# Optimization experiments

Hardware: AMD Instinct MI355X
Metric: run time of the kernel (lower is better)

The kernel has to match this reference:

```python
import jax, jax.numpy as jnp
import numpy as np

TOP_K = 2


def setup_inputs() -> dict:
    key = jax.random.key(0)
    ks = jax.random.split(key, 5)
    B, N, C, FF, E = 2, 2048, 1024, 4096, 8
    x = jax.random.normal(ks[0], (B, N, C), dtype=jnp.float32)
    router_w = jax.random.normal(ks[1], (E, C), dtype=jnp.float32) * 0.02
    # xavier-uniform-like init for expert weights
    lim1 = np.sqrt(6.0 / (FF + C))
    expert_w1 = jax.random.uniform(ks[2], (E, FF, C), dtype=jnp.float32, minval=-lim1, maxval=lim1)
    expert_b1 = jnp.zeros((E, FF), dtype=jnp.float32)
    expert_w2 = jax.random.uniform(ks[3], (E, C, FF), dtype=jnp.float32, minval=-lim1, maxval=lim1)
    expert_b2 = jnp.zeros((E, C), dtype=jnp.float32)
    return {"x": x, "router_w": router_w, "expert_w1": expert_w1,
            "expert_b1": expert_b1, "expert_w2": expert_w2, "expert_b2": expert_b2}


def reference(x, router_w, expert_w1, expert_b1, expert_w2, expert_b2):
    # x: [B,N,C]; router_w: [E,C]; expert_w1: [E,FF,C]; expert_w2: [E,C,FF]
    router_logits = jnp.einsum('bnc,ec->bne', x, router_w)          # [B,N,E]
    router_probs = jax.nn.softmax(router_logits, axis=-1)
    expert_weights, expert_idx = jax.lax.top_k(router_probs, TOP_K)  # [B,N,K]
    expert_weights = expert_weights / (expert_weights.sum(axis=-1, keepdims=True) + 1e-9)
    # Dense all-expert FFN (avoids materializing per-token gathered weight matrices)
    h = jnp.einsum('bnc,efc->bnef', x, expert_w1) + expert_b1        # [B,N,E,FF]
    h = jax.nn.gelu(h, approximate=False)                            # torch nn.GELU = exact
    out_all = jnp.einsum('bnef,ecf->bnec', h, expert_w2) + expert_b2  # [B,N,E,C]
    # Gather top-k expert outputs and combine
    out_k = jnp.take_along_axis(out_all, expert_idx[..., None], axis=2)  # [B,N,K,C]
    return (out_k * expert_weights[..., None]).sum(axis=2)           # [B,N,C]
```

## Files before the change

### kernel.cpp

```cpp
#include <hip/hip_runtime.h>
#include <hip/hip_bf16.h>
#include <cstdint>

#define TTOK  4096
#define CDIM  1024
#define FFDIM 4096
#define NEXP  8


typedef short short8 __attribute__((ext_vector_type(8)));
typedef float f32x4 __attribute__((ext_vector_type(4)));

__device__ __forceinline__ unsigned short f2bf(float f) {
    unsigned int u = __float_as_uint(f);
    u = u + 0x7fffu + ((u >> 16) & 1u);
    return (unsigned short)(u >> 16);
}

__device__ __forceinline__ void gl_lds16(const unsigned short* g, unsigned short* l) {
    __builtin_amdgcn_global_load_lds(
        (const __attribute__((address_space(1))) unsigned int*)g,
        (__attribute__((address_space(3))) unsigned int*)l, 16, 0, 0);
}

__device__ __forceinline__ int swz_off(int row, int kq) {
    const int line = row >> 1;
    const int cp = ((((row & 1) << 2) | kq) ^ (line & 7));
    return line * 64 + cp * 8;
}

#define SBAR() do { __builtin_amdgcn_sched_barrier(0); \
                    __builtin_amdgcn_s_barrier();      \
                    __builtin_amdgcn_sched_barrier(0); } while (0)

__global__ void cast_kernel(const float* __restrict__ src, unsigned short* __restrict__ dst) {
    int i = blockIdx.x * blockDim.x + threadIdx.x;
    float4 v = reinterpret_cast<const float4*>(src)[i];
    ushort4 o;
    o.x = f2bf(v.x); o.y = f2bf(v.y); o.z = f2bf(v.z); o.w = f2bf(v.w);
    reinterpret_cast<ushort4*>(dst)[i] = o;
}

__global__ void router_kernel(const float* __restrict__ x, const float* __restrict__ rw,
                              int* __restrict__ counts, int* __restrict__ btok,
                              float* __restrict__ bgate) {
    const int wave = threadIdx.x >> 6;
    const int lane = threadIdx.x & 63;
    const int t = blockIdx.x * 4 + wave;
    const float* xr = x + (size_t)t * CDIM;

    float acc[NEXP];
#pragma unroll
    for (int e = 0; e < NEXP; e++) acc[e] = 0.f;
    for (int c = lane; c < CDIM; c += 64) {
        float xv = xr[c];
#pragma unroll
        for (int e = 0; e < NEXP; e++) acc[e] += xv * rw[e * CDIM + c];
    }
#pragma unroll
    for (int e = 0; e < NEXP; e++) {
#pragma unroll
        for (int off = 32; off > 0; off >>= 1) acc[e] += __shfl_down(acc[e], off, 64);
    }
    if (lane == 0) {
        float mx = acc[0];
#pragma unroll
        for (int e = 1; e < NEXP; e++) mx = fmaxf(mx, acc[e]);
        float p[NEXP]; float s = 0.f;
#pragma unroll
        for (int e = 0; e < NEXP; e++) { p[e] = expf(acc[e] - mx); s += p[e]; }
        int i0 = 0;
#pragma unroll
        for (int e = 1; e < NEXP; e++) if (p[e] > p[i0]) i0 = e;
        int i1 = (i0 == 0) ? 1 : 0;
#pragma unroll
        for (int e = 0; e < NEXP; e++) if (e != i0 && p[e] > p[i1]) i1 = e;
        float pr0 = p[i0] / s, pr1 = p[i1] / s;
        float rs = 1.f / (pr0 + pr1 + 1e-9f);
        float w0 = pr0 * rs, w1 = pr1 * rs;
        int pos = atomicAdd(&counts[i0], 1);
        btok[i0 * TTOK + pos] = t; bgate[i0 * TTOK + pos] = w0;
        pos = atomicAdd(&counts[i1], 1);
        btok[i1 * TTOK + pos] = t; bgate[i1 * TTOK + pos] = w1;
    }
}

__global__ void offsets_kernel(const int* __restrict__ counts, int* __restrict__ offsets) {
    if (threadIdx.x == 0 && blockIdx.x == 0) {
        int s = 0;
        for (int e = 0; e < NEXP; e++) { offsets[e] = s; s += counts[e]; }
        offsets[NEXP] = s;
    }
}


__global__ __launch_bounds__(512, 2) void gemm1p_kernel(
    const unsigned short* __restrict__ xb, const unsigned short* __restrict__ w1b,
    const float* __restrict__ b1, const int* __restrict__ counts,
    const int* __restrict__ offsets, const int* __restrict__ btok,
    unsigned short* __restrict__ H) {
    const int e = blockIdx.z;
    const int cnt = counts[e];
    const int m0 = blockIdx.y * 256;
    if (m0 >= cnt) return;
    const int n0 = blockIdx.x * 256;
    const int po = offsets[e];
    const int NT = CDIM / 32;

    __shared__ uint4 smem4[8192];
    unsigned short* S = (unsigned short*)smem4;

    const int tid = threadIdx.x;
    const int wid = tid >> 6, lane = tid & 63;
    const int lm = lane & 15, kq = lane >> 4;
    const int wr = wid >> 2, wc = wid & 3;

    const int sline = tid >> 3;
    const int c128s = (tid & 7) ^ (sline & 7);
    const int prty  = c128s >> 2;
    const int skc   = (c128s & 3) << 3;
    const int ar0 = min(m0 + (sline << 1) + prty, cnt - 1);
    const int ar1 = min(m0 + 128 + (sline << 1) + prty, cnt - 1);
    const unsigned short* asrc0 = xb + (size_t)btok[e * TTOK + ar0] * CDIM + skc;
    const unsigned short* asrc1 = xb + (size_t)btok[e * TTOK + ar1] * CDIM + skc;
    const unsigned short* bsrc0 = w1b + ((size_t)e * FFDIM + n0 + (sline << 1) + prty) * CDIM + skc;
    const unsigned short* bsrc1 = bsrc0 + (size_t)128 * CDIM;

    int offA[8], offB[4];
#pragma unroll
    for (int f = 0; f < 8; f++) offA[f] = swz_off(wr * 128 + f * 16 + lm, kq);
#pragma unroll
    for (int g = 0; g < 4; g++) offB[g] = swz_off(wc * 64 + g * 16 + lm, kq);

    f32x4 acc[8][4];
#pragma unroll
    for (int f = 0; f < 8; f++)
#pragma unroll
        for (int g = 0; g < 4; g++) { f32x4 z = {0.f, 0.f, 0.f, 0.f}; acc[f][g] = z; }

#pragma unroll
    for (int tt = 0; tt < 3; tt++) {
        unsigned short* Sa = S + tt * 16384;
        unsigned short* Sb = Sa + 8192;
        const int ko = tt * 32;
        gl_lds16(asrc0 + ko, Sa + tid * 8);
        gl_lds16(bsrc0 + ko, Sb + tid * 8);
        gl_lds16(asrc1 + ko, Sa + (512 + tid) * 8);
        gl_lds16(bsrc1 + ko, Sb + (512 + tid) * 8);
    }
    asm volatile("s_waitcnt vmcnt(8)" ::: "memory");
    SBAR();

    for (int t = 0; t < NT; ++t) {
        unsigned short* Ab = S + (t & 3) * 16384;
        unsigned short* Bb = Ab + 8192;
        int ts = t + 3; if (ts >= NT) ts -= NT;
        unsigned short* Sa = S + (ts & 3) * 16384;
        unsigned short* Sb = Sa + 8192;
        const int ko = ts * 32;

        short8 bf[4];
        {
            short8 af[4];
#pragma unroll
            for (int f = 0; f < 4; f++) af[f] = *reinterpret_cast<const short8*>(&Ab[offA[f]]);
#pragma unroll
            for (int g = 0; g < 4; g++) bf[g] = *reinterpret_cast<const short8*>(&Bb[offB[g]]);
            gl_lds16(asrc0 + ko, Sa + tid * 8);
            gl_lds16(bsrc0 + ko, Sb + tid * 8);
            SBAR();
            __builtin_amdgcn_s_setprio(1);
#pragma unroll
            for (int f = 0; f < 4; f++)
#pragma unroll
                for (int g = 0; g < 4; g++)
                    acc[f][g] = __builtin_amdgcn_mfma_f32_16x16x32_bf16(af[f], bf[g], acc[f][g], 0, 0, 0);
            __builtin_amdgcn_s_setprio(0);
            SBAR();
        }
        {
            short8 af[4];
#pragma unroll
            for (int f = 0; f < 4; f++) af[f] = *reinterpret_cast<const short8*>(&Ab[offA[4 + f]]);
            gl_lds16(asrc1 + ko, Sa + (512 + tid) * 8);
            gl_lds16(bsrc1 + ko, Sb + (512 + tid) * 8);
            asm volatile("s_waitcnt vmcnt(8)" ::: "memory");
            SBAR();
            __builtin_amdgcn_s_setprio(1);
#pragma unroll
            for (int f = 0; f < 4; f++)
#pragma unroll
                for (int g = 0; g < 4; g++)
                    acc[4 + f][g] = __builtin_amdgcn_mfma_f32_16x16x32_bf16(af[f], bf[g], acc[4 + f][g], 0, 0, 0);
            __builtin_amdgcn_s_setprio(0);
            SBAR();
        }
    }

    asm volatile("s_waitcnt vmcnt(0)" ::: "memory");
    __syncthreads();

    float bias[4];
#pragma unroll
    for (int g = 0; g < 4; g++) bias[g] = b1[e * FFDIM + n0 + wc * 64 + g * 16 + lm];

    unsigned short* Cs = S;
#pragma unroll
    for (int f = 0; f < 8; f++) {
#pragma unroll
        for (int r = 0; r < 4; r++) {
            const int row = wr * 128 + f * 16 + kq * 4 + r;
#pragma unroll
            for (int g = 0; g < 4; g++) {
                const int col = wc * 64 + g * 16 + lm;
                float h = acc[f][g][r] + bias[g];
                float gl = 0.5f * h * (1.f + erff(h * 0.70710678118654752f));
                Cs[(row * 256 + col) ^ ((row & 7) << 3)] = f2bf(gl);
            }
        }
    }
    __syncthreads();
#pragma unroll
    for (int q = 0; q < 16; q++) {
        const int cq = q * 512 + tid;
        const int row = cq >> 5;
        const int cc = cq & 31;
        const int mrow = m0 + row;
        if (mrow < cnt)
            *reinterpret_cast<uint4*>(&H[(size_t)(po + mrow) * FFDIM + n0 + cc * 8]) =
                *reinterpret_cast<const uint4*>(&Cs[(row * 256 + cc * 8) ^ ((row & 7) << 3)]);
    }
}

__global__ __launch_bounds__(512, 2) void gemm2p_kernel(
    const unsigned short* __restrict__ H, const unsigned short* __restrict__ w2b,
    const float* __restrict__ b2, const int* __restrict__ counts,
    const int* __restrict__ offsets, const int* __restrict__ btok,
    const float* __restrict__ bgate, float* __restrict__ out) {
    const int e = blockIdx.z;
    const int cnt = counts[e];
    const int m0 = (blockIdx.y >> 1) * 256;
    const int ks = blockIdx.y & 1;
    if (m0 >= cnt) return;
    const int n0 = blockIdx.x * 256;
    const int po = offsets[e];
    const int NT = 2048 / 32;

    __shared__ uint4 smem4[8192];
    unsigned short* S = (unsigned short*)smem4;

    const int tid = threadIdx.x;
    const int wid = tid >> 6, lane = tid & 63;
    const int lm = lane & 15, kq = lane >> 4;
    const int wr = wid >> 2, wc = wid & 3;

    const int sline = tid >> 3;
    const int c128s = (tid & 7) ^ (sline & 7);
    const int prty  = c128s >> 2;
    const int skc   = (c128s & 3) << 3;
    const int koff  = ks * 2048;
    const int ar0 = min(m0 + (sline << 1) + prty, cnt - 1);
    const int ar1 = min(m0 + 128 + (sline << 1) + prty, cnt - 1);
    const unsigned short* asrc0 = H + (size_t)(po + ar0) * FFDIM + koff + skc;
    const unsigned short* asrc1 = H + (size_t)(po + ar1) * FFDIM + koff + skc;
    const unsigned short* bsrc0 = w2b + ((size_t)e * CDIM + n0 + (sline << 1) + prty) * FFDIM + koff + skc;
    const unsigned short* bsrc1 = bsrc0 + (size_t)128 * FFDIM;

    int offA[8], offB[4];
#pragma unroll
    for (int f = 0; f < 8; f++) offA[f] = swz_off(wr * 128 + f * 16 + lm, kq);
#pragma unroll
    for (int g = 0; g < 4; g++) offB[g] = swz_off(wc * 64 + g * 16 + lm, kq);

    f32x4 acc[8][4];
#pragma unroll
    for (int f = 0; f < 8; f++)
#pragma unroll
        for (int g = 0; g < 4; g++) { f32x4 z = {0.f, 0.f, 0.f, 0.f}; acc[f][g] = z; }

#pragma unroll
    for (int tt = 0; tt < 3; tt++) {
        unsigned short* Sa = S + tt * 16384;
        unsigned short* Sb = Sa + 8192;
        const int ko = tt * 32;
        gl_lds16(asrc0 + ko, Sa + tid * 8);
        gl_lds16(bsrc0 + ko, Sb + tid * 8);
        gl_lds16(asrc1 + ko, Sa + (512 + tid) * 8);
        gl_lds16(bsrc1 + ko, Sb + (512 + tid) * 8);
    }
    asm volatile("s_waitcnt vmcnt(8)" ::: "memory");
    SBAR();

    for (int t = 0; t < NT; ++t) {
        unsigned short* Ab = S + (t & 3) * 16384;
        unsigned short* Bb = Ab + 8192;
        int ts = t + 3; if (ts >= NT) ts -= NT;
        unsigned short* Sa = S + (ts & 3) * 16384;
        unsigned short* Sb = Sa + 8192;
        const int ko = ts * 32;

        short8 bf[4];
        {
            short8 af[4];
#pragma unroll
            for (int f = 0; f < 4; f++) af[f] = *reinterpret_cast<const short8*>(&Ab[offA[f]]);
#pragma unroll
            for (int g = 0; g < 4; g++) bf[g] = *reinterpret_cast<const short8*>(&Bb[offB[g]]);
            gl_lds16(asrc0 + ko, Sa + tid * 8);
            gl_lds16(bsrc0 + ko, Sb + tid * 8);
            SBAR();
            __builtin_amdgcn_s_setprio(1);
#pragma unroll
            for (int f = 0; f < 4; f++)
#pragma unroll
                for (int g = 0; g < 4; g++)
                    acc[f][g] = __builtin_amdgcn_mfma_f32_16x16x32_bf16(af[f], bf[g], acc[f][g], 0, 0, 0);
            __builtin_amdgcn_s_setprio(0);
            SBAR();
        }
        {
            short8 af[4];
#pragma unroll
            for (int f = 0; f < 4; f++) af[f] = *reinterpret_cast<const short8*>(&Ab[offA[4 + f]]);
            gl_lds16(asrc1 + ko, Sa + (512 + tid) * 8);
            gl_lds16(bsrc1 + ko, Sb + (512 + tid) * 8);
            asm volatile("s_waitcnt vmcnt(8)" ::: "memory");
            SBAR();
            __builtin_amdgcn_s_setprio(1);
#pragma unroll
            for (int f = 0; f < 4; f++)
#pragma unroll
                for (int g = 0; g < 4; g++)
                    acc[4 + f][g] = __builtin_amdgcn_mfma_f32_16x16x32_bf16(af[f], bf[g], acc[4 + f][g], 0, 0, 0);
            __builtin_amdgcn_s_setprio(0);
            SBAR();
        }
    }

    asm volatile("s_waitcnt vmcnt(0)" ::: "memory");

    float bias[4];
#pragma unroll
    for (int g = 0; g < 4; g++)
        bias[g] = (ks == 0) ? b2[e * CDIM + n0 + wc * 64 + g * 16 + lm] : 0.f;

#pragma unroll
    for (int f = 0; f < 8; f++) {
#pragma unroll
        for (int r = 0; r < 4; r++) {
            const int mrow = m0 + wr * 128 + f * 16 + kq * 4 + r;
            if (mrow < cnt) {
                const int tok = btok[e * TTOK + mrow];
                const float g8 = bgate[e * TTOK + mrow];
                float* orow = out + (size_t)tok * CDIM + n0;
#pragma unroll
                for (int g = 0; g < 4; g++)
                    atomicAdd(orow + wc * 64 + g * 16 + lm, g8 * (acc[f][g][r] + bias[g]));
            }
        }
    }
}


__global__ __launch_bounds__(256) void gemm1_kernel(
    const unsigned short* __restrict__ xb, const float* __restrict__ w1,
    const float* __restrict__ b1, const int* __restrict__ counts,
    const int* __restrict__ offsets, const int* __restrict__ btok,
    unsigned short* __restrict__ H) {
    const int e = blockIdx.z;
    const int cnt = counts[e];
    const int m0 = blockIdx.y * 128;
    if (m0 >= cnt) return;
    const int n0 = blockIdx.x * 128;
    const int po = offsets[e];

    __shared__ unsigned short As[128][32];
    __shared__ unsigned short Bs[128][32];

    const int tid = threadIdx.x;
    const int wave = tid >> 6, lane = tid & 63;
    const int wm = (wave >> 1) << 6, wn = (wave & 1) << 6;
    const int lm = lane & 15, kq = lane >> 4;

    f32x4 acc[4][4];
#pragma unroll
    for (int i = 0; i < 4; i++)
#pragma unroll
        for (int j = 0; j < 4; j++) { f32x4 z = {0.f, 0.f, 0.f, 0.f}; acc[i][j] = z; }

    const float* w1e = w1 + (size_t)e * FFDIM * CDIM;
    const int arow = tid >> 1;
    const int acolb = (tid & 1) * 16;
    int tokA = -1;
    if (m0 + arow < cnt) tokA = btok[e * TTOK + m0 + arow];
    const int brow = tid >> 1;
    const int bcol = (tid & 1) * 16;

    for (int k0 = 0; k0 < CDIM; k0 += 32) {
        uint4 a0 = {0, 0, 0, 0}, a1 = {0, 0, 0, 0};
        if (tokA >= 0) {
            const uint4* src = reinterpret_cast<const uint4*>(xb + (size_t)tokA * CDIM + k0 + acolb);
            a0 = src[0]; a1 = src[1];
        }
        *reinterpret_cast<uint4*>(&As[arow][acolb]) = a0;
        *reinterpret_cast<uint4*>(&As[arow][acolb + 8]) = a1;
        {
            const float* src = w1e + (size_t)(n0 + brow) * CDIM + k0 + bcol;
            ushort4* dst = reinterpret_cast<ushort4*>(&Bs[brow][bcol]);
#pragma unroll
            for (int q = 0; q < 4; q++) {
                float4 v = reinterpret_cast<const float4*>(src)[q];
                ushort4 o; o.x = f2bf(v.x); o.y = f2bf(v.y); o.z = f2bf(v.z); o.w = f2bf(v.w);
                dst[q] = o;
            }
        }
        __syncthreads();
        short8 af[4], bfr[4];
#pragma unroll
        for (int i = 0; i < 4; i++) af[i] = *reinterpret_cast<const short8*>(&As[wm + i * 16 + lm][kq * 8]);
#pragma unroll
        for (int j = 0; j < 4; j++) bfr[j] = *reinterpret_cast<const short8*>(&Bs[wn + j * 16 + lm][kq * 8]);
#pragma unroll
        for (int i = 0; i < 4; i++)
#pragma unroll
            for (int j = 0; j < 4; j++)
                acc[i][j] = __builtin_amdgcn_mfma_f32_16x16x32_bf16(af[i], bfr[j], acc[i][j], 0, 0, 0);
        __syncthreads();
    }

#pragma unroll
    for (int j = 0; j < 4; j++) {
        const int fcol = n0 + wn + j * 16 + lm;
        const float bias = b1[e * FFDIM + fcol];
#pragma unroll
        for (int i = 0; i < 4; i++) {
#pragma unroll
            for (int r = 0; r < 4; r++) {
                const int mrow = m0 + wm + i * 16 + kq * 4 + r;
                if (mrow < cnt) {
                    float h = acc[i][j][r] + bias;
                    float g = 0.5f * h * (1.f + erff(h * 0.70710678118654752f));
                    H[(size_t)(po + mrow) * FFDIM + fcol] = f2bf(g);
                }
            }
        }
    }
}

__global__ __launch_bounds__(256) void gemm2_kernel(
    const unsigned short* __restrict__ H, const float* __restrict__ w2,
    const float* __restrict__ b2, const int* __restrict__ counts,
    const int* __restrict__ offsets, const int* __restrict__ btok,
    const float* __restrict__ bgate, float* __restrict__ out) {
    const int e = blockIdx.z;
    const int cnt = counts[e];
    const int m0 = blockIdx.y * 128;
    if (m0 >= cnt) return;
    const int n0 = blockIdx.x * 128;
    const int po = offsets[e];

    __shared__ unsigned short As[128][32];
    __shared__ unsigned short Bs[128][32];

    const int tid = threadIdx.x;
    const int wave = tid >> 6, lane = tid & 63;
    const int wm = (wave >> 1) << 6, wn = (wave & 1) << 6;
    const int lm = lane & 15, kq = lane >> 4;

    f32x4 acc[4][4];
#pragma unroll
    for (int i = 0; i < 4; i++)
#pragma unroll
        for (int j = 0; j < 4; j++) { f32x4 z = {0.f, 0.f, 0.f, 0.f}; acc[i][j] = z; }

    const float* w2e = w2 + (size_t)e * CDIM * FFDIM;
    const int arow = tid >> 1;
    const int acolb = (tid & 1) * 16;
    const bool aval = (m0 + arow < cnt);
    const unsigned short* asrc = H + (size_t)(po + m0 + arow) * FFDIM + acolb;
    const int brow = tid >> 1;
    const int bcol = (tid & 1) * 16;

    for (int k0 = 0; k0 < FFDIM; k0 += 32) {
        uint4 a0 = {0, 0, 0, 0}, a1 = {0, 0, 0, 0};
        if (aval) {
            const uint4* src = reinterpret_cast<const uint4*>(asrc + k0);
            a0 = src[0]; a1 = src[1];
        }
        *reinterpret_cast<uint4*>(&As[arow][acolb]) = a0;
        *reinterpret_cast<uint4*>(&As[arow][acolb + 8]) = a1;
        {
            const float* src = w2e + (size_t)(n0 + brow) * FFDIM + k0 + bcol;
            ushort4* dst = reinterpret_cast<ushort4*>(&Bs[brow][bcol]);
#pragma unroll
            for (int q = 0; q < 4; q++) {
                float4 v = reinterpret_cast<const float4*>(src)[q];
                ushort4 o; o.x = f2bf(v.x); o.y = f2bf(v.y); o.z = f2bf(v.z); o.w = f2bf(v.w);
                dst[q] = o;
            }
        }
        __syncthreads();
        short8 af[4], bfr[4];
#pragma unroll
        for (int i = 0; i < 4; i++) af[i] = *reinterpret_cast<const short8*>(&As[wm + i * 16 + lm][kq * 8]);
#pragma unroll
        for (int j = 0; j < 4; j++) bfr[j] = *reinterpret_cast<const short8*>(&Bs[wn + j * 16 + lm][kq * 8]);
#pragma unroll
        for (int i = 0; i < 4; i++)
#pragma unroll
            for (int j = 0; j < 4; j++)
                acc[i][j] = __builtin_amdgcn_mfma_f32_16x16x32_bf16(af[i], bfr[j], acc[i][j], 0, 0, 0);
        __syncthreads();
    }

    float bias[4];
#pragma unroll
    for (int j = 0; j < 4; j++) bias[j] = b2[e * CDIM + n0 + wn + j * 16 + lm];

#pragma unroll
    for (int i = 0; i < 4; i++) {
#pragma unroll
        for (int r = 0; r < 4; r++) {
            const int mrow = m0 + wm + i * 16 + kq * 4 + r;
            if (mrow < cnt) {
                const int tok = btok[e * TTOK + mrow];
                const float g = bgate[e * TTOK + mrow];
                float* orow = out + (size_t)tok * CDIM;
#pragma unroll
                for (int j = 0; j < 4; j++) {
                    const int c = n0 + wn + j * 16 + lm;
                    atomicAdd(orow + c, g * (acc[i][j][r] + bias[j]));
                }
            }
        }
    }
}

extern "C" void kernel_launch(void* const* d_in, const int* in_sizes, int n_in,
                              void* d_out, int out_size, void* d_ws, size_t ws_size,
                              hipStream_t stream) {
    const float* x  = (const float*)d_in[0];
    const float* rw = (const float*)d_in[1];
    const float* w1 = (const float*)d_in[2];
    const float* b1 = (const float*)d_in[3];
    const float* w2 = (const float*)d_in[4];
    const float* b2 = (const float*)d_in[5];
    float* out = (float*)d_out;

    char* ws = (char*)d_ws;
    int*   counts  = (int*)ws;
    int*   offsets = (int*)(ws + 64);
    int*   btok    = (int*)(ws + 4096);
    float* bgate   = (float*)(ws + 4096 + 131072);

    hipMemsetAsync(d_out, 0, (size_t)out_size * sizeof(float), stream);
    hipMemsetAsync(counts, 0, 64, stream);

    const bool fast = ws_size >= ((size_t)137 << 20);

    if (fast) {
        unsigned short* xb = (unsigned short*)(ws + ((size_t)1 << 20));
        unsigned short* Wb = (unsigned short*)(ws + ((size_t)9 << 20));
        unsigned short* H  = (unsigned short*)(ws + ((size_t)73 << 20));

        cast_kernel<<<(TTOK * CDIM) / (256 * 4), 256, 0, stream>>>(x, xb);
        router_kernel<<<TTOK / 4, 256, 0, stream>>>(x, rw, counts, btok, bgate);
        offsets_kernel<<<1, 64, 0, stream>>>(counts, offsets);
        cast_kernel<<<(NEXP * FFDIM * CDIM) / (256 * 4), 256, 0, stream>>>(w1, Wb);
        gemm1p_kernel<<<dim3(FFDIM / 256, TTOK / 256, NEXP), 512, 0, stream>>>(
            xb, Wb, b1, counts, offsets, btok, H);
        cast_kernel<<<(NEXP * CDIM * FFDIM) / (256 * 4), 256, 0, stream>>>(w2, Wb);
        gemm2p_kernel<<<dim3(CDIM / 256, (TTOK / 256) * 2, NEXP), 512, 0, stream>>>(
            H, Wb, b2, counts, offsets, btok, bgate, out);
    } else {
        unsigned short* xb = (unsigned short*)(ws + ((size_t)1 << 20));
        unsigned short* H  = (unsigned short*)(ws + ((size_t)16 << 20));

        cast_kernel<<<(TTOK * CDIM) / (256 * 4), 256, 0, stream>>>(x, xb);
        router_kernel<<<TTOK / 4, 256, 0, stream>>>(x, rw, counts, btok, bgate);
        offsets_kernel<<<1, 64, 0, stream>>>(counts, offsets);
        gemm1_kernel<<<dim3(FFDIM / 128, TTOK / 128, NEXP), 256, 0, stream>>>(
            xb, w1, b1, counts, offsets, btok, H);
        gemm2_kernel<<<dim3(CDIM / 128, TTOK / 128, NEXP), 256, 0, stream>>>(
            H, w2, b2, counts, offsets, btok, bgate, out);
    }
}
```

Baseline: 709.2 us.

## Restructure MoE GEMM pipelines to double-buffered 64-wide K tiles

Both expert GEMM kernels move from a 4-stage ring of 32-wide K tiles to a 2-stage double buffer of 64-wide K tiles. Each outer iteration now runs four MFMA sub-phases, with explicit lgkmcnt waits replacing some barriers. The aim is fewer barriers and loop iterations per unit of K work and larger loads in flight. The trade-off is a shallower prefetch distance, which may expose more global-load latency.

Measured after the change: 688.4 us. 2.9% less time.

```diff
diff --git a/kernel.cpp b/kernel.cpp
--- a/kernel.cpp
+++ b/kernel.cpp
@@ -32,6 +32,8 @@
 #define SBAR() do { __builtin_amdgcn_sched_barrier(0); \
                     __builtin_amdgcn_s_barrier();      \
                     __builtin_amdgcn_sched_barrier(0); } while (0)
+#define LGKM0() do { asm volatile("s_waitcnt lgkmcnt(0)" ::: "memory"); \
+                     __builtin_amdgcn_sched_barrier(0); } while (0)
 
 __global__ void cast_kernel(const float* __restrict__ src, unsigned short* __restrict__ dst) {
     int i = blockIdx.x * blockDim.x + threadIdx.x;
@@ -94,7 +96,7 @@
 }
 
 
-__global__ __launch_bounds__(512, 2) void gemm1p_kernel(
+__global__ __launch_bounds__(512, 2) void gemm1p8_kernel(
     const unsigned short* __restrict__ xb, const unsigned short* __restrict__ w1b,
     const float* __restrict__ b1, const int* __restrict__ counts,
     const int* __restrict__ offsets, const int* __restrict__ btok,
@@ -105,7 +107,7 @@
     if (m0 >= cnt) return;
     const int n0 = blockIdx.x * 256;
     const int po = offsets[e];
-    const int NT = CDIM / 32;
+    const int NT = CDIM / 64;
 
     __shared__ uint4 smem4[8192];
     unsigned short* S = (unsigned short*)smem4;
@@ -119,12 +121,13 @@
     const int c128s = (tid & 7) ^ (sline & 7);
     const int prty  = c128s >> 2;
     const int skc   = (c128s & 3) << 3;
-    const int ar0 = min(m0 + (sline << 1) + prty, cnt - 1);
-    const int ar1 = min(m0 + 128 + (sline << 1) + prty, cnt - 1);
-    const unsigned short* asrc0 = xb + (size_t)btok[e * TTOK + ar0] * CDIM + skc;
-    const unsigned short* asrc1 = xb + (size_t)btok[e * TTOK + ar1] * CDIM + skc;
-    const unsigned short* bsrc0 = w1b + ((size_t)e * FFDIM + n0 + (sline << 1) + prty) * CDIM + skc;
-    const unsigned short* bsrc1 = bsrc0 + (size_t)128 * CDIM;
+    const int rowLo = (sline << 1) + prty;
+    const int tokLo = btok[e * TTOK + min(m0 + rowLo, cnt - 1)];
+    const int tokHi = btok[e * TTOK + min(m0 + 128 + rowLo, cnt - 1)];
+    const unsigned short* aLo = xb + (size_t)tokLo * CDIM + skc;
+    const unsigned short* aHi = xb + (size_t)tokHi * CDIM + skc;
+    const unsigned short* bLo = w1b + ((size_t)e * FFDIM + n0 + rowLo) * CDIM + skc;
+    const unsigned short* bHi = bLo + (size_t)128 * CDIM;
 
     int offA[8], offB[4];
 #pragma unroll
@@ -138,61 +141,91 @@
 #pragma unroll
         for (int g = 0; g < 4; g++) { f32x4 z = {0.f, 0.f, 0.f, 0.f}; acc[f][g] = z; }
 
-#pragma unroll
-    for (int tt = 0; tt < 3; tt++) {
-        unsigned short* Sa = S + tt * 16384;
-        unsigned short* Sb = Sa + 8192;
-        const int ko = tt * 32;
-        gl_lds16(asrc0 + ko, Sa + tid * 8);
-        gl_lds16(bsrc0 + ko, Sb + tid * 8);
-        gl_lds16(asrc1 + ko, Sa + (512 + tid) * 8);
-        gl_lds16(bsrc1 + ko, Sb + (512 + tid) * 8);
-    }
-    asm volatile("s_waitcnt vmcnt(8)" ::: "memory");
+    gl_lds16(aLo,      S + tid * 8);
+    gl_lds16(aHi,      S + 4096 + tid * 8);
+    gl_lds16(bLo,      S + 16384 + tid * 8);
+    gl_lds16(bHi,      S + 16384 + 4096 + tid * 8);
+    gl_lds16(aLo + 32, S + 8192 + tid * 8);
+    gl_lds16(aHi + 32, S + 8192 + 4096 + tid * 8);
+    gl_lds16(bLo + 32, S + 24576 + tid * 8);
+    gl_lds16(bHi + 32, S + 24576 + 4096 + tid * 8);
+    asm volatile("s_waitcnt vmcnt(4)" ::: "memory");
     SBAR();
 
     for (int t = 0; t < NT; ++t) {
-        unsigned short* Ab = S + (t & 3) * 16384;
-        unsigned short* Bb = Ab + 8192;
-        int ts = t + 3; if (ts >= NT) ts -= NT;
-        unsigned short* Sa = S + (ts & 3) * 16384;
-        unsigned short* Sb = Sa + 8192;
-        const int ko = ts * 32;
-
-        short8 bf[4];
-        {
-            short8 af[4];
-#pragma unroll
-            for (int f = 0; f < 4; f++) af[f] = *reinterpret_cast<const short8*>(&Ab[offA[f]]);
-#pragma unroll
-            for (int g = 0; g < 4; g++) bf[g] = *reinterpret_cast<const short8*>(&Bb[offB[g]]);
-            gl_lds16(asrc0 + ko, Sa + tid * 8);
-            gl_lds16(bsrc0 + ko, Sb + tid * 8);
-            SBAR();
-            __builtin_amdgcn_s_setprio(1);
-#pragma unroll
-            for (int f = 0; f < 4; f++)
-#pragma unroll
-                for (int g = 0; g < 4; g++)
-                    acc[f][g] = __builtin_amdgcn_mfma_f32_16x16x32_bf16(af[f], bf[g], acc[f][g], 0, 0, 0);
-            __builtin_amdgcn_s_setprio(0);
-            SBAR();
-        }
-        {
-            short8 af[4];
-#pragma unroll
-            for (int f = 0; f < 4; f++) af[f] = *reinterpret_cast<const short8*>(&Ab[offA[4 + f]]);
-            gl_lds16(asrc1 + ko, Sa + (512 + tid) * 8);
-            gl_lds16(bsrc1 + ko, Sb + (512 + tid) * 8);
-            asm volatile("s_waitcnt vmcnt(8)" ::: "memory");
-            SBAR();
-            __builtin_amdgcn_s_setprio(1);
-#pragma unroll
-            for (int f = 0; f < 4; f++)
-#pragma unroll
-                for (int g = 0; g < 4; g++)
-                    acc[4 + f][g] = __builtin_amdgcn_mfma_f32_16x16x32_bf16(af[f], bf[g], acc[4 + f][g], 0, 0, 0);
-            __builtin_amdgcn_s_setprio(0);
+        unsigned short* Cb = S + (t & 1) * 32768;
+        unsigned short* Nb = S + ((t & 1) ^ 1) * 32768;
+        const int ts = (t + 1 == NT) ? 0 : t + 1;
+        const int g0 = ts * 64;
+        short8 bfr[4];
+        {
+            short8 af[4];
+#pragma unroll
+            for (int f = 0; f < 4; f++) af[f] = *reinterpret_cast<const short8*>(&Cb[offA[f]]);
+#pragma unroll
+            for (int g = 0; g < 4; g++) bfr[g] = *reinterpret_cast<const short8*>(&Cb[16384 + offB[g]]);
+            gl_lds16(aLo + g0, Nb + tid * 8);
+            gl_lds16(aHi + g0, Nb + 4096 + tid * 8);
+            LGKM0();
+            __builtin_amdgcn_s_setprio(1);
+#pragma unroll
+            for (int f = 0; f < 4; f++)
+#pragma unroll
+                for (int g = 0; g < 4; g++)
+                    acc[f][g] = __builtin_amdgcn_mfma_f32_16x16x32_bf16(af[f], bfr[g], acc[f][g], 0, 0, 0);
+            __builtin_amdgcn_s_setprio(0);
+            SBAR();
+        }
+        {
+            short8 af[4];
+#pragma unroll
+            for (int f = 0; f < 4; f++) af[f] = *reinterpret_cast<const short8*>(&Cb[offA[4 + f]]);
+            gl_lds16(bLo + g0, Nb + 16384 + tid * 8);
+            gl_lds16(bHi + g0, Nb + 16384 + 4096 + tid * 8);
+            LGKM0();
+            __builtin_amdgcn_s_setprio(1);
+#pragma unroll
+            for (int f = 0; f < 4; f++)
+#pragma unroll
+                for (int g = 0; g < 4; g++)
+                    acc[4 + f][g] = __builtin_amdgcn_mfma_f32_16x16x32_bf16(af[f], bfr[g], acc[4 + f][g], 0, 0, 0);
+            __builtin_amdgcn_s_setprio(0);
+            asm volatile("s_waitcnt vmcnt(4)" ::: "memory");
+            SBAR();
+        }
+        {
+            short8 af[4];
+#pragma unroll
+            for (int f = 0; f < 4; f++) af[f] = *reinterpret_cast<const short8*>(&Cb[8192 + offA[f]]);
+#pragma unroll
+            for (int g = 0; g < 4; g++) bfr[g] = *reinterpret_cast<const short8*>(&Cb[24576 + offB[g]]);
+            gl_lds16(aLo + g0 + 32, Nb + 8192 + tid * 8);
+            gl_lds16(aHi + g0 + 32, Nb + 8192 + 4096 + tid * 8);
+            LGKM0();
+            __builtin_amdgcn_s_setprio(1);
+#pragma unroll
+            for (int f = 0; f < 4; f++)
+#pragma unroll
+                for (int g = 0; g < 4; g++)
+                    acc[f][g] = __builtin_amdgcn_mfma_f32_16x16x32_bf16(af[f], bfr[g], acc[f][g], 0, 0, 0);
+            __builtin_amdgcn_s_setprio(0);
+            SBAR();
+        }
+        {
+            short8 af[4];
+#pragma unroll
+            for (int f = 0; f < 4; f++) af[f] = *reinterpret_cast<const short8*>(&Cb[8192 + offA[4 + f]]);
+            gl_lds16(bLo + g0 + 32, Nb + 24576 + tid * 8);
+            gl_lds16(bHi + g0 + 32, Nb + 24576 + 4096 + tid * 8);
+            LGKM0();
+            __builtin_amdgcn_s_setprio(1);
+#pragma unroll
+            for (int f = 0; f < 4; f++)
+#pragma unroll
+                for (int g = 0; g < 4; g++)
+                    acc[4 + f][g] = __builtin_amdgcn_mfma_f32_16x16x32_bf16(af[f], bfr[g], acc[4 + f][g], 0, 0, 0);
+            __builtin_amdgcn_s_setprio(0);
+            asm volatile("s_waitcnt vmcnt(4)" ::: "memory");
             SBAR();
         }
     }
@@ -232,7 +265,7 @@
     }
 }
 
-__global__ __launch_bounds__(512, 2) void gemm2p_kernel(
+__global__ __launch_bounds__(512, 2) void gemm2p8_kernel(
     const unsigned short* __restrict__ H, const unsigned short* __restrict__ w2b,
     const float* __restrict__ b2, const int* __restrict__ counts,
     const int* __restrict__ offsets, const int* __restrict__ btok,
@@ -244,7 +277,7 @@
     if (m0 >= cnt) return;
     const int n0 = blockIdx.x * 256;
     const int po = offsets[e];
-    const int NT = 2048 / 32;
+    const int NT = 2048 / 64;
 
     __shared__ uint4 smem4[8192];
     unsigned short* S = (unsigned short*)smem4;
@@ -258,13 +291,14 @@
     const int c128s = (tid & 7) ^ (sline & 7);
     const int prty  = c128s >> 2;
     const int skc   = (c128s & 3) << 3;
+    const int rowLo = (sline << 1) + prty;
     const int koff  = ks * 2048;
-    const int ar0 = min(m0 + (sline << 1) + prty, cnt - 1);
-    const int ar1 = min(m0 + 128 + (sline << 1) + prty, cnt - 1);
-    const unsigned short* asrc0 = H + (size_t)(po + ar0) * FFDIM + koff + skc;
-    const unsigned short* asrc1 = H + (size_t)(po + ar1) * FFDIM + koff + skc;
-    const unsigned short* bsrc0 = w2b + ((size_t)e * CDIM + n0 + (sline << 1) + prty) * FFDIM + koff + skc;
-    const unsigned short* bsrc1 = bsrc0 + (size_t)128 * FFDIM;
+    const int rLo = min(m0 + rowLo, cnt - 1);
+    const int rHi = min(m0 + 128 + rowLo, cnt - 1);
+    const unsigned short* aLo = H + (size_t)(po + rLo) * FFDIM + koff + skc;
+    const unsigned short* aHi = H + (size_t)(po + rHi) * FFDIM + koff + skc;
+    const unsigned short* bLo = w2b + ((size_t)e * CDIM + n0 + rowLo) * FFDIM + koff + skc;
+    const unsigned short* bHi = bLo + (size_t)128 * FFDIM;
 
     int offA[8], offB[4];
 #pragma unroll
@@ -278,61 +312,91 @@
 #pragma unroll
         for (int g = 0; g < 4; g++) { f32x4 z = {0.f, 0.f, 0.f, 0.f}; acc[f][g] = z; }
 
-#pragma unroll
-    for (int tt = 0; tt < 3; tt++) {
-        unsigned short* Sa = S + tt * 16384;
-        unsigned short* Sb = Sa + 8192;
-        const int ko = tt * 32;
-        gl_lds16(asrc0 + ko, Sa + tid * 8);
-        gl_lds16(bsrc0 + ko, Sb + tid * 8);
-        gl_lds16(asrc1 + ko, Sa + (512 + tid) * 8);
-        gl_lds16(bsrc1 + ko, Sb + (512 + tid) * 8);
-    }
-    asm volatile("s_waitcnt vmcnt(8)" ::: "memory");
+    gl_lds16(aLo,      S + tid * 8);
+    gl_lds16(aHi,      S + 4096 + tid * 8);
+    gl_lds16(bLo,      S + 16384 + tid * 8);
+    gl_lds16(bHi,      S + 16384 + 4096 + tid * 8);
+    gl_lds16(aLo + 32, S + 8192 + tid * 8);
+    gl_lds16(aHi + 32, S + 8192 + 4096 + tid * 8);
+    gl_lds16(bLo + 32, S + 24576 + tid * 8);
+    gl_lds16(bHi + 32, S + 24576 + 4096 + tid * 8);
+    asm volatile("s_waitcnt vmcnt(4)" ::: "memory");
     SBAR();
 
     for (int t = 0; t < NT; ++t) {
-        unsigned short* Ab = S + (t & 3) * 16384;
-        unsigned short* Bb = Ab + 8192;
-        int ts = t + 3; if (ts >= NT) ts -= NT;
-        unsigned short* Sa = S + (ts & 3) * 16384;
-        unsigned short* Sb = Sa + 8192;
-        const int ko = ts * 32;
-
-        short8 bf[4];
-        {
-            short8 af[4];
-#pragma unroll
-            for (int f = 0; f < 4; f++) af[f] = *reinterpret_cast<const short8*>(&Ab[offA[f]]);
-#pragma unroll
-            for (int g = 0; g < 4; g++) bf[g] = *reinterpret_cast<const short8*>(&Bb[offB[g]]);
-            gl_lds16(asrc0 + ko, Sa + tid * 8);
-            gl_lds16(bsrc0 + ko, Sb + tid * 8);
-            SBAR();
-            __builtin_amdgcn_s_setprio(1);
-#pragma unroll
-            for (int f = 0; f < 4; f++)
-#pragma unroll
-                for (int g = 0; g < 4; g++)
-                    acc[f][g] = __builtin_amdgcn_mfma_f32_16x16x32_bf16(af[f], bf[g], acc[f][g], 0, 0, 0);
-            __builtin_amdgcn_s_setprio(0);
-            SBAR();
-        }
-        {
-            short8 af[4];
-#pragma unroll
-            for (int f = 0; f < 4; f++) af[f] = *reinterpret_cast<const short8*>(&Ab[offA[4 + f]]);
-            gl_lds16(asrc1 + ko, Sa + (512 + tid) * 8);
-            gl_lds16(bsrc1 + ko, Sb + (512 + tid) * 8);
-            asm volatile("s_waitcnt vmcnt(8)" ::: "memory");
-            SBAR();
-            __builtin_amdgcn_s_setprio(1);
-#pragma unroll
-            for (int f = 0; f < 4; f++)
-#pragma unroll
-                for (int g = 0; g < 4; g++)
-                    acc[4 + f][g] = __builtin_amdgcn_mfma_f32_16x16x32_bf16(af[f], bf[g], acc[4 + f][g], 0, 0, 0);
-            __builtin_amdgcn_s_setprio(0);
+        unsigned short* Cb = S + (t & 1) * 32768;
+        unsigned short* Nb = S + ((t & 1) ^ 1) * 32768;
+        const int ts = (t + 1 == NT) ? 0 : t + 1;
+        const int g0 = ts * 64;
+        short8 bfr[4];
+        {
+            short8 af[4];
+#pragma unroll
+            for (int f = 0; f < 4; f++) af[f] = *reinterpret_cast<const short8*>(&Cb[offA[f]]);
+#pragma unroll
+            for (int g = 0; g < 4; g++) bfr[g] = *reinterpret_cast<const short8*>(&Cb[16384 + offB[g]]);
+            gl_lds16(aLo + g0, Nb + tid * 8);
+            gl_lds16(aHi + g0, Nb + 4096 + tid * 8);
+            LGKM0();
+            __builtin_amdgcn_s_setprio(1);
+#pragma unroll
+            for (int f = 0; f < 4; f++)
+#pragma unroll
+                for (int g = 0; g < 4; g++)
+                    acc[f][g] = __builtin_amdgcn_mfma_f32_16x16x32_bf16(af[f], bfr[g], acc[f][g], 0, 0, 0);
+            __builtin_amdgcn_s_setprio(0);
+            SBAR();
+        }
+        {
+            short8 af[4];
+#pragma unroll
+            for (int f = 0; f < 4; f++) af[f] = *reinterpret_cast<const short8*>(&Cb[offA[4 + f]]);
+            gl_lds16(bLo + g0, Nb + 16384 + tid * 8);
+            gl_lds16(bHi + g0, Nb + 16384 + 4096 + tid * 8);
+            LGKM0();
+            __builtin_amdgcn_s_setprio(1);
+#pragma unroll
+            for (int f = 0; f < 4; f++)
+#pragma unroll
+                for (int g = 0; g < 4; g++)
+                    acc[4 + f][g] = __builtin_amdgcn_mfma_f32_16x16x32_bf16(af[f], bfr[g], acc[4 + f][g], 0, 0, 0);
+            __builtin_amdgcn_s_setprio(0);
+            asm volatile("s_waitcnt vmcnt(4)" ::: "memory");
+            SBAR();
+        }
+        {
+            short8 af[4];
+#pragma unroll
+            for (int f = 0; f < 4; f++) af[f] = *reinterpret_cast<const short8*>(&Cb[8192 + offA[f]]);
+#pragma unroll
+            for (int g = 0; g < 4; g++) bfr[g] = *reinterpret_cast<const short8*>(&Cb[24576 + offB[g]]);
+            gl_lds16(aLo + g0 + 32, Nb + 8192 + tid * 8);
+            gl_lds16(aHi + g0 + 32, Nb + 8192 + 4096 + tid * 8);
+            LGKM0();
+            __builtin_amdgcn_s_setprio(1);
+#pragma unroll
+            for (int f = 0; f < 4; f++)
+#pragma unroll
+                for (int g = 0; g < 4; g++)
+                    acc[f][g] = __builtin_amdgcn_mfma_f32_16x16x32_bf16(af[f], bfr[g], acc[f][g], 0, 0, 0);
+            __builtin_amdgcn_s_setprio(0);
+            SBAR();
+        }
+        {
+            short8 af[4];
+#pragma unroll
+            for (int f = 0; f < 4; f++) af[f] = *reinterpret_cast<const short8*>(&Cb[8192 + offA[4 + f]]);
+            gl_lds16(bLo + g0 + 32, Nb + 24576 + tid * 8);
+            gl_lds16(bHi + g0 + 32, Nb + 24576 + 4096 + tid * 8);
+            LGKM0();
+            __builtin_amdgcn_s_setprio(1);
+#pragma unroll
+            for (int f = 0; f < 4; f++)
+#pragma unroll
+                for (int g = 0; g < 4; g++)
+                    acc[4 + f][g] = __builtin_amdgcn_mfma_f32_16x16x32_bf16(af[f], bfr[g], acc[4 + f][g], 0, 0, 0);
+            __builtin_amdgcn_s_setprio(0);
+            asm volatile("s_waitcnt vmcnt(4)" ::: "memory");
             SBAR();
         }
     }
@@ -567,10 +631,10 @@
         router_kernel<<<TTOK / 4, 256, 0, stream>>>(x, rw, counts, btok, bgate);
         offsets_kernel<<<1, 64, 0, stream>>>(counts, offsets);
         cast_kernel<<<(NEXP * FFDIM * CDIM) / (256 * 4), 256, 0, stream>>>(w1, Wb);
-        gemm1p_kernel<<<dim3(FFDIM / 256, TTOK / 256, NEXP), 512, 0, stream>>>(
+        gemm1p8_kernel<<<dim3(FFDIM / 256, TTOK / 256, NEXP), 512, 0, stream>>>(
             xb, Wb, b1, counts, offsets, btok, H);
         cast_kernel<<<(NEXP * CDIM * FFDIM) / (256 * 4), 256, 0, stream>>>(w2, Wb);
-        gemm2p_kernel<<<dim3(CDIM / 256, (TTOK / 256) * 2, NEXP), 512, 0, stream>>>(
+        gemm2p8_kernel<<<dim3(CDIM / 256, (TTOK / 256) * 2, NEXP), 512, 0, stream>>>(
             H, Wb, b2, counts, offsets, btok, bgate, out);
     } else {
         unsigned short* xb = (unsigned short*)(ws + ((size_t)1 << 20));
```
